# Performance work log

Hardware: AMD Instinct MI355X
Metric: run time of the kernel (lower is better)

## Reference

```python
import jax, jax.numpy as jnp
import numpy as np

CUTOFF = 5.0
EPS = 1e-3  # keras BatchNormalization default epsilon
L = 3       # num_interactions
N = 100000
E = 1600000
H = 64
FIN = 16


def setup_inputs() -> dict:
    key = jax.random.key(0)
    ks = jax.random.split(key, 16)
    s = 0.1  # weight scale for numerical stability
    return {
        "x": jax.random.normal(ks[0], (N, FIN), jnp.float32),
        "edge_index": jax.random.randint(ks[1], (2, E), 0, N, jnp.int32),
        "distances": jax.random.uniform(ks[2], (E,), jnp.float32) * CUTOFF,
        "edge_attr": jax.random.normal(ks[3], (E, 1), jnp.float32),
        "emb_W": jax.random.normal(ks[4], (FIN, H), jnp.float32) * s,
        "emb_b": jnp.zeros((H,), jnp.float32),
        "fW1": jax.random.normal(ks[5], (L, 1, H), jnp.float32) * s,
        "fb1": jnp.zeros((L, H), jnp.float32),
        "fW2": jax.random.normal(ks[6], (L, H, H), jnp.float32) * s,
        "fb2": jnp.zeros((L, H), jnp.float32),
        "iW1": jax.random.normal(ks[7], (L, H, H), jnp.float32) * s,
        "ib1": jnp.zeros((L, H), jnp.float32),
        "iW2": jax.random.normal(ks[8], (L, H, H), jnp.float32) * s,
        "ib2": jnp.zeros((L, H), jnp.float32),
        "bn_gamma": jnp.ones((L, H), jnp.float32),
        "bn_beta": jnp.zeros((L, H), jnp.float32),
        "oW1": jax.random.normal(ks[9], (H, H // 2), jnp.float32) * s,
        "ob1": jnp.zeros((H // 2,), jnp.float32),
        "og1": jnp.ones((H // 2,), jnp.float32),
        "obt1": jnp.zeros((H // 2,), jnp.float32),
        "oW2": jax.random.normal(ks[10], (H // 2, H // 2), jnp.float32) * s,
        "ob2": jnp.zeros((H // 2,), jnp.float32),
        "og2": jnp.ones((H // 2,), jnp.float32),
        "obt2": jnp.zeros((H // 2,), jnp.float32),
        "fin_W": jax.random.normal(ks[11], (H // 2, 3), jnp.float32) * s,
        "fin_b": jnp.zeros((3,), jnp.float32),
    }


def reference(x, edge_index, distances, edge_attr,
              emb_W, emb_b, fW1, fb1, fW2, fb2,
              iW1, ib1, iW2, ib2, bn_gamma, bn_beta,
              oW1, ob1, og1, obt1, oW2, ob2, og2, obt2,
              fin_W, fin_b):
    n_nodes = x.shape[0]
    row, col = edge_index[0], edge_index[1]
    inv = 1.0 / jnp.sqrt(1.0 + EPS)  # BN inference with moving mean=0, var=1

    # shared edge-level quantities
    scaled = distances * (2.0 / CUTOFF) - 1.0                       # [E]
    cut = 0.5 * (jnp.cos(distances * np.pi / CUTOFF) + 1.0)
    cut = jnp.where(distances <= CUTOFF, cut, 0.0)                  # [E]

    h = x @ emb_W + emb_b                                           # [N,H]
    for l in range(L):
        # filter MLP: [E,1] -> [E,F]
        f = jnp.tanh(scaled[:, None] * fW1[l][0] + fb1[l]) @ fW2[l] + fb2[l]
        f = f * cut[:, None]
        # original: sum_F(neighbor[:,None,:] * f[:,:,None]) == neighbor * sum_F(f)
        fs = f.sum(-1)                                              # [E]
        msgs = h[col] * fs[:, None]                                 # [E,H] gather
        agg = jax.ops.segment_sum(msgs, row, num_segments=n_nodes)  # [N,H] scatter-add
        out = jax.nn.softplus(agg @ iW1[l] + ib1[l]) @ iW2[l] + ib2[l]
        out = out * inv * bn_gamma[l] + bn_beta[l]                  # BN (inference)
        h = h + out

    g = h.mean(axis=0)                                              # [H]
    g = jax.nn.softplus(g @ oW1 + ob1) * inv * og1 + obt1
    g = jax.nn.softplus(g @ oW2 + ob2) * inv * og2 + obt2
    return g @ fin_W + fin_b                                        # [3]
```

## Files before the change

kernel.cpp:

```cpp
#include <hip/hip_runtime.h>
#include <hip/hip_fp16.h>
#include <math.h>

#define CUTOFF 5.0f
#define H 64
#define FIN 16
#define NLAYERS 3
#define LUTN 2048
#define LUTSTRIDE 2052
#define ASTRIDE 72
#define MEANB 256
#define BROWS 512
#define NBMAX 256
#define MAXC 10240
#define ABLK 4096

#define BN_INV 0.999500374750f

typedef _Float16 h8 __attribute__((ext_vector_type(8)));
typedef _Float16 h2 __attribute__((ext_vector_type(2)));
typedef float f32x4 __attribute__((ext_vector_type(4)));
typedef unsigned int u32x2 __attribute__((ext_vector_type(2)));

__device__ __forceinline__ float softplus_f(float x) {
    return fmaxf(x, 0.f) + __logf(1.f + __expf(-fabsf(x)));
}

__global__ __launch_bounds__(1024)
void k_pre(const float* __restrict__ x, const float* __restrict__ emb_W,
           const float* __restrict__ emb_b, _Float16* __restrict__ h0,
           const float* __restrict__ fW1, const float* __restrict__ fb1,
           const float* __restrict__ fW2, const float* __restrict__ fb2,
           const float* __restrict__ iW1, const float* __restrict__ iW2,
           const float* __restrict__ bn_g, const float* __restrict__ bn_b,
           const float* __restrict__ ib2, h8* __restrict__ Wsw,
           float* __restrict__ b2p, float* __restrict__ lut,
           unsigned int* __restrict__ cursor, int N, int nbE16) {
    __shared__ float swsum[64];
    __shared__ float sbsum;
    int b = blockIdx.x;
    int t = threadIdx.x;
    if (b < nbE16) {
        int lane = t & 63;
        int w = t >> 6;
        int node = b * 16 + w;
        if (node < N) {
            float acc = emb_b[lane];
#pragma unroll
            for (int k = 0; k < FIN; k++) acc += x[node * FIN + k] * emb_W[k * H + lane];
            h0[(size_t)node * H + lane] = (_Float16)acc;
        }
    } else if (b < nbE16 + NLAYERS * 3) {
        int lb = b - nbE16;
        int l = lb / 3, part = lb % 3;
        if (t < 64) {
            float s = 0.f;
            for (int j = 0; j < H; j++) s += fW2[l * H * H + t * H + j];
            swsum[t] = s;
        }
        if (t == 64) {
            float s = 0.f;
            for (int j = 0; j < H; j++) s += fb2[l * H + j];
            sbsum = s;
        }
        __syncthreads();
        int i = part * 1024 + t;
        if (i <= LUTN) {
            float d = (float)i * (CUTOFF / (float)LUTN);
            float scaled = d * (2.0f / CUTOFF) - 1.0f;
            float cut = 0.5f * (__cosf(d * (3.14159265358979f / CUTOFF)) + 1.0f);
            if (d > CUTOFF) cut = 0.f;
            float s = 0.f;
            for (int hh = 0; hh < H; hh++) {
                int wi = l * H + hh;
                s += tanhf(scaled * fW1[wi] + fb1[wi]) * swsum[hh];
            }
            lut[l * LUTSTRIDE + i] = cut * (s + sbsum);
        }
    } else {
        int tid = (b - nbE16 - NLAYERS * 3) * 1024 + t;
        if (tid < NBMAX) cursor[tid] = (unsigned)tid * MAXC;
        if (tid < NLAYERS * H)
            b2p[tid] = ib2[tid] * BN_INV * bn_g[tid] + bn_b[tid];
        if (tid < NLAYERS * 2 * 8 * 64) {
            int lane = tid & 63;
            int frag = (tid >> 6) & 7;
            int mat  = (tid >> 9) & 1;
            int l    = tid >> 10;
            int kt = frag >> 2, nt = frag & 3;
            int n = nt * 16 + (lane & 15);
            int k0 = kt * 32 + (lane >> 4) * 8;
            const float* W = (mat ? iW2 : iW1) + l * H * H;
            float scale = mat ? BN_INV * bn_g[l * H + n] : 1.0f;
            h8 v;
#pragma unroll
            for (int j = 0; j < 8; j++) v[j] = (_Float16)(W[(k0 + j) * H + n] * scale);
            Wsw[tid] = v;
        }
    }
}

__global__ __launch_bounds__(1024)
void k_passA(const int* __restrict__ ei, const float* __restrict__ dist,
             unsigned int* __restrict__ cursor, u32x2* __restrict__ stg,
             int N, int E, int NB) {
    __shared__ unsigned s_cnt[NBMAX];
    __shared__ unsigned s_base[NBMAX];
    int t = threadIdx.x;
    int e0 = blockIdx.x * ABLK;
    for (int i = t; i < NB; i += 1024) s_cnt[i] = 0;
    __syncthreads();
    int rowv[4];
    unsigned rkv[4] = {0u, 0u, 0u, 0u};
    int bkv[4] = {0, 0, 0, 0};
#pragma unroll
    for (int j = 0; j < 4; j++) {
        int e = e0 + j * 1024 + t;
        rowv[j] = -1;
        if (e < E) {
            int r = ei[e];
            int bk = r / BROWS;
            rkv[j] = atomicAdd(&s_cnt[bk], 1u);
            bkv[j] = bk;
            rowv[j] = r;
        }
    }
    __syncthreads();
    for (int i = t; i < NB; i += 1024)
        s_base[i] = s_cnt[i] ? atomicAdd(&cursor[i], s_cnt[i]) : 0u;
    __syncthreads();
#pragma unroll
    for (int j = 0; j < 4; j++) {
        int e = e0 + j * 1024 + t;
        if (e < E) {
            int col = ei[E + e];
            float d = dist[e];
            int didx = (int)(d * (32768.0f / CUTOFF) + 0.5f);
            didx = max(0, min(didx, 32767));
            unsigned g = s_base[bkv[j]] + rkv[j];
            u32x2 rec;
            rec.x = ((unsigned)col << 15) | (unsigned)didx;
            rec.y = (unsigned)rowv[j];
            if (g < ((unsigned)bkv[j] + 1u) * MAXC)
                stg[g] = rec;
        }
    }
}

__global__ __launch_bounds__(1024)
void k_passB(const u32x2* __restrict__ stg, const unsigned int* __restrict__ cursor,
             int* __restrict__ row_ptr, unsigned int* __restrict__ recs,
             int N, int NB) {
    __shared__ int s_bb[NBMAX];
    __shared__ int s_c[BROWS];
    __shared__ int s_x[BROWS];
    __shared__ unsigned s_out[MAXC];
    int b = blockIdx.x, t = threadIdx.x;
    if (t < NBMAX) {
        int cb = 0;
        if (t < NB) {
            cb = (int)(cursor[t] - (unsigned)t * MAXC);
            cb = min(cb, MAXC);
        }
        s_bb[t] = cb;
    }
    __syncthreads();
    for (int off = 1; off < NBMAX; off <<= 1) {
        int v = 0;
        if (t < NBMAX && t >= off) v = s_bb[t - off];
        __syncthreads();
        if (t < NBMAX) s_bb[t] += v;
        __syncthreads();
    }
    int bbase = (b > 0) ? s_bb[b - 1] : 0;
    int cnt = s_bb[b] - bbase;
    int r0 = b * BROWS;
    int r1 = min(r0 + BROWS, N);
    int nrows = r1 - r0;
    if (t < BROWS) s_c[t] = 0;
    __syncthreads();
    const u32x2* mystg = stg + (size_t)b * MAXC;
    for (int i = t; i < cnt; i += 1024)
        atomicAdd(&s_c[(int)mystg[i].y - r0], 1);
    __syncthreads();
    if (t < BROWS) s_x[t] = s_c[t];
    __syncthreads();
    for (int off = 1; off < BROWS; off <<= 1) {
        int v = 0;
        if (t < BROWS && t >= off) v = s_x[t - off];
        __syncthreads();
        if (t < BROWS) s_x[t] += v;
        __syncthreads();
    }
    if (t < nrows) {
        int excl = s_x[t] - s_c[t];
        row_ptr[r0 + t] = bbase + excl;
        s_c[t] = excl;
    }
    if (b == NB - 1 && t == 0) row_ptr[N] = bbase + cnt;
    __syncthreads();
    for (int i = t; i < cnt; i += 1024) {
        u32x2 rec = mystg[i];
        int slot = atomicAdd(&s_c[(int)rec.y - r0], 1);
        s_out[slot] = rec.x;
    }
    __syncthreads();
    for (int i = t; i < cnt; i += 1024)
        recs[bbase + i] = s_out[i];
}

__global__ __launch_bounds__(256, 8)
void k_layer(const int* __restrict__ row_ptr, const unsigned int* __restrict__ recs,
             const float* __restrict__ lutl, const h8* __restrict__ Wsw,
             const float* __restrict__ b1, const float* __restrict__ b2p,
             const _Float16* __restrict__ h_in, _Float16* __restrict__ h_out,
             int N) {
    __shared__ float s_lut[LUTN + 1];
    __shared__ _Float16 sA[64 * ASTRIDE];
    for (int i = threadIdx.x; i <= LUTN; i += 256) s_lut[i] = lutl[i];
    __syncthreads();

    int lane = threadIdx.x & 63;
    int w = threadIdx.x >> 6;
    int base = blockIdx.x * 64 + w * 16;
    int g = lane >> 3, ci = lane & 7;
    const uint4* h4 = (const uint4*)h_in;

#pragma unroll
    for (int half = 0; half < 2; half++) {
        int node = base + half * 8 + g;
        h2 acc[4];
#pragma unroll
        for (int q = 0; q < 4; q++) acc[q] = (h2){(_Float16)0.f, (_Float16)0.f};
        if (node < N) {
            int s = row_ptr[node], t = row_ptr[node + 1];
            for (int k = s; k < t; k += 4) {
                int k1 = (k + 1 < t) ? k + 1 : k;
                int k2 = (k + 2 < t) ? k + 2 : k;
                int k3 = (k + 3 < t) ? k + 3 : k;
                unsigned r0 = recs[k];
                unsigned r1 = recs[k1];
                unsigned r2 = recs[k2];
                unsigned r3 = recs[k3];
                float td0 = (float)(r0 & 32767u) * (1.0f / 16.0f);
                float td1 = (float)(r1 & 32767u) * (1.0f / 16.0f);
                float td2 = (float)(r2 & 32767u) * (1.0f / 16.0f);
                float td3 = (float)(r3 & 32767u) * (1.0f / 16.0f);
                int i0 = (int)td0, i1 = (int)td1, i2 = (int)td2, i3 = (int)td3;
                float fr0 = td0 - (float)i0, fr1 = td1 - (float)i1;
                float fr2 = td2 - (float)i2, fr3 = td3 - (float)i3;
                float f00 = s_lut[i0], f01 = s_lut[i1];
                float f02 = s_lut[i2], f03 = s_lut[i3];
                float fv0 = f00 + fr0 * (s_lut[i0 + 1] - f00);
                float fv1 = f01 + fr1 * (s_lut[i1 + 1] - f01);
                float fv2 = f02 + fr2 * (s_lut[i2 + 1] - f02);
                float fv3 = f03 + fr3 * (s_lut[i3 + 1] - f03);
                fv1 = (k + 1 < t) ? fv1 : 0.f;
                fv2 = (k + 2 < t) ? fv2 : 0.f;
                fv3 = (k + 3 < t) ? fv3 : 0.f;
                union { uint4 u; h2 v[4]; } p0, p1, p2, p3;
                p0.u = h4[(r0 >> 15) * 8u + (unsigned)ci];
                p1.u = h4[(r1 >> 15) * 8u + (unsigned)ci];
                p2.u = h4[(r2 >> 15) * 8u + (unsigned)ci];
                p3.u = h4[(r3 >> 15) * 8u + (unsigned)ci];
                _Float16 fh0 = (_Float16)fv0, fh1 = (_Float16)fv1;
                _Float16 fh2 = (_Float16)fv2, fh3 = (_Float16)fv3;
                h2 a0 = (h2){fh0, fh0};
                h2 a1 = (h2){fh1, fh1};
                h2 a2 = (h2){fh2, fh2};
                h2 a3 = (h2){fh3, fh3};
#pragma unroll
                for (int q = 0; q < 4; q++) acc[q] += a0 * p0.v[q];
#pragma unroll
                for (int q = 0; q < 4; q++) acc[q] += a1 * p1.v[q];
#pragma unroll
                for (int q = 0; q < 4; q++) acc[q] += a2 * p2.v[q];
#pragma unroll
                for (int q = 0; q < 4; q++) acc[q] += a3 * p3.v[q];
            }
        }
        union { uint4 u4; h2 v[4]; } pk;
#pragma unroll
        for (int q = 0; q < 4; q++) pk.v[q] = acc[q];
        *(uint4*)&sA[(size_t)(w * 16 + half * 8 + g) * ASTRIDE + ci * 8] = pk.u4;
    }

    int q4 = lane >> 4, c16 = lane & 15;
    int rowb = w * 16;
    const h8* WB1 = Wsw;
    const h8* WB2 = Wsw + 8 * 64;
    h8 A0 = *(const h8*)&sA[(size_t)(rowb + c16) * ASTRIDE + q4 * 8];
    h8 A1 = *(const h8*)&sA[(size_t)(rowb + c16) * ASTRIDE + 32 + q4 * 8];
    f32x4 C1[4];
#pragma unroll
    for (int nt = 0; nt < 4; nt++) {
        f32x4 c = {0.f, 0.f, 0.f, 0.f};
        c = __builtin_amdgcn_mfma_f32_16x16x32_f16(A0, WB1[nt * 64 + lane], c, 0, 0, 0);
        c = __builtin_amdgcn_mfma_f32_16x16x32_f16(A1, WB1[(4 + nt) * 64 + lane], c, 0, 0, 0);
        C1[nt] = c;
    }
#pragma unroll
    for (int nt = 0; nt < 4; nt++) {
        float bb = b1[nt * 16 + c16];
#pragma unroll
        for (int reg = 0; reg < 4; reg++) {
            float v = softplus_f(C1[nt][reg] + bb);
            sA[(size_t)(rowb + q4 * 4 + reg) * ASTRIDE + nt * 16 + c16] = (_Float16)v;
        }
    }
    h8 M0 = *(const h8*)&sA[(size_t)(rowb + c16) * ASTRIDE + q4 * 8];
    h8 M1 = *(const h8*)&sA[(size_t)(rowb + c16) * ASTRIDE + 32 + q4 * 8];
    f32x4 C2[4];
#pragma unroll
    for (int nt = 0; nt < 4; nt++) {
        f32x4 c = {0.f, 0.f, 0.f, 0.f};
        c = __builtin_amdgcn_mfma_f32_16x16x32_f16(M0, WB2[nt * 64 + lane], c, 0, 0, 0);
        c = __builtin_amdgcn_mfma_f32_16x16x32_f16(M1, WB2[(4 + nt) * 64 + lane], c, 0, 0, 0);
        C2[nt] = c;
    }
#pragma unroll
    for (int nt = 0; nt < 4; nt++) {
        float bb2 = b2p[nt * 16 + c16];
#pragma unroll
        for (int reg = 0; reg < 4; reg++) {
            int node = base + q4 * 4 + reg;
            if (node < N) {
                size_t idx = (size_t)node * H + nt * 16 + c16;
                float hn = (float)h_in[idx] + C2[nt][reg] + bb2;
                h_out[idx] = (_Float16)hn;
            }
        }
    }
}

__global__ __launch_bounds__(256)
void k_mean(const _Float16* __restrict__ hb, float* __restrict__ partials, int N) {
    __shared__ float s_r[4][H];
    int lane = threadIdx.x & 63;
    int w = threadIdx.x >> 6;
    int wg = blockIdx.x * 4 + w;
    int stride = gridDim.x * 4;
    float local = 0.f;
    for (int i = wg; i < N; i += stride) local += (float)hb[(size_t)i * H + lane];
    s_r[w][lane] = local;
    __syncthreads();
    if (w == 0) {
        float s = s_r[0][lane] + s_r[1][lane] + s_r[2][lane] + s_r[3][lane];
        partials[(size_t)blockIdx.x * H + lane] = s;
    }
}

__global__ __launch_bounds__(256)
void k_final(const float* __restrict__ partials, int N,
             const float* __restrict__ oW1, const float* __restrict__ ob1,
             const float* __restrict__ og1, const float* __restrict__ obt1,
             const float* __restrict__ oW2, const float* __restrict__ ob2,
             const float* __restrict__ og2, const float* __restrict__ obt2,
             const float* __restrict__ fin_W, const float* __restrict__ fin_b,
             float* __restrict__ out) {
    __shared__ float red[4][H];
    __shared__ float sg[H], su[H / 2], sv[H / 2];
    int t = threadIdx.x;
    int ch = t & 63, grp = t >> 6;
    float s = 0.f;
    for (int b = grp; b < MEANB; b += 4) s += partials[(size_t)b * H + ch];
    red[grp][ch] = s;
    __syncthreads();
    if (t < H) sg[t] = (red[0][t] + red[1][t] + red[2][t] + red[3][t]) / (float)N;
    __syncthreads();
    int j = t;
    if (j < H / 2) {
        float acc = ob1[j];
        for (int k = 0; k < H; k++) acc += sg[k] * oW1[k * (H / 2) + j];
        su[j] = softplus_f(acc) * BN_INV * og1[j] + obt1[j];
    }
    __syncthreads();
    if (j < H / 2) {
        float acc = ob2[j];
        for (int k = 0; k < H / 2; k++) acc += su[k] * oW2[k * (H / 2) + j];
        sv[j] = softplus_f(acc) * BN_INV * og2[j] + obt2[j];
    }
    __syncthreads();
    if (j < 3) {
        float acc = fin_b[j];
        for (int k = 0; k < H / 2; k++) acc += sv[k] * fin_W[k * 3 + j];
        out[j] = acc;
    }
}

extern "C" void kernel_launch(void* const* d_in, const int* in_sizes, int n_in,
                              void* d_out, int out_size, void* d_ws, size_t ws_size,
                              hipStream_t stream) {
    const float* x      = (const float*)d_in[0];
    const int*   ei     = (const int*)d_in[1];
    const float* dist   = (const float*)d_in[2];
    const float* emb_W  = (const float*)d_in[4];
    const float* emb_b  = (const float*)d_in[5];
    const float* fW1    = (const float*)d_in[6];
    const float* fb1    = (const float*)d_in[7];
    const float* fW2    = (const float*)d_in[8];
    const float* fb2    = (const float*)d_in[9];
    const float* iW1    = (const float*)d_in[10];
    const float* ib1    = (const float*)d_in[11];
    const float* iW2    = (const float*)d_in[12];
    const float* ib2    = (const float*)d_in[13];
    const float* bn_g   = (const float*)d_in[14];
    const float* bn_b   = (const float*)d_in[15];
    const float* oW1    = (const float*)d_in[16];
    const float* ob1    = (const float*)d_in[17];
    const float* og1    = (const float*)d_in[18];
    const float* obt1   = (const float*)d_in[19];
    const float* oW2    = (const float*)d_in[20];
    const float* ob2    = (const float*)d_in[21];
    const float* og2    = (const float*)d_in[22];
    const float* obt2   = (const float*)d_in[23];
    const float* fin_W  = (const float*)d_in[24];
    const float* fin_b  = (const float*)d_in[25];
    float* out = (float*)d_out;

    int N = in_sizes[0] / FIN;
    int E = in_sizes[2];
    int NB = (N + BROWS - 1) / BROWS;

    float*  ws   = (float*)d_ws;
    _Float16* h0 = (_Float16*)ws;
    _Float16* h1 = h0 + (size_t)N * H;
    unsigned int* recs = (unsigned int*)(h1 + (size_t)N * H);
    h8*     Wsw  = (h8*)(recs + E);
    float*  lut  = (float*)(Wsw + NLAYERS * 2 * 8 * 64);
    float*  partials = lut + 3 * LUTSTRIDE;
    float*  b2p  = partials + MEANB * H;
    u32x2*  stg  = (u32x2*)(b2p + NLAYERS * H);
    int*    row_ptr = (int*)(stg + (size_t)NBMAX * MAXC);
    unsigned int* cursor = (unsigned int*)(row_ptr + N + 1);

    int nbE16 = (N + 15) / 16;
    int nb_pre = nbE16 + NLAYERS * 3 + 3;
    k_pre<<<nb_pre, 1024, 0, stream>>>(x, emb_W, emb_b, h0,
                                       fW1, fb1, fW2, fb2, iW1, iW2,
                                       bn_g, bn_b, ib2, Wsw, b2p, lut,
                                       cursor, N, nbE16);

    int nbA = (E + ABLK - 1) / ABLK;
    k_passA<<<nbA, 1024, 0, stream>>>(ei, dist, cursor, stg, N, E, NB);
    k_passB<<<NB, 1024, 0, stream>>>(stg, cursor, row_ptr, recs, N, NB);

    _Float16* hp[2] = {h0, h1};
    int nb_tile = (N + 63) / 64;
    for (int l = 0; l < NLAYERS; l++) {
        k_layer<<<nb_tile, 256, 0, stream>>>(row_ptr, recs, lut + (size_t)l * LUTSTRIDE,
                                             Wsw + (size_t)l * 1024,
                                             ib1 + l * H, b2p + l * H,
                                             hp[l & 1], hp[(l + 1) & 1], N);
    }
    _Float16* h_final = hp[NLAYERS & 1];

    k_mean<<<MEANB, 256, 0, stream>>>(h_final, partials, N);
    k_final<<<1, 256, 0, stream>>>(partials, N, oW1, ob1, og1, obt1,
                                   oW2, ob2, og2, obt2, fin_W, fin_b, out);
}
```

Before: 339.1 us.

## Fuse edge bucketing into pre kernel, interleave node gathers, fuse final-layer mean

```diff
diff --git a/kernel.cpp b/kernel.cpp
--- a/kernel.cpp
+++ b/kernel.cpp
@@ -35,23 +35,66 @@
            const float* __restrict__ bn_g, const float* __restrict__ bn_b,
            const float* __restrict__ ib2, h8* __restrict__ Wsw,
            float* __restrict__ b2p, float* __restrict__ lut,
-           unsigned int* __restrict__ cursor, int N, int nbE16) {
+           const int* __restrict__ ei, const float* __restrict__ dist,
+           unsigned int* __restrict__ cursor, u32x2* __restrict__ stg,
+           int N, int E, int NB, int nbA, int nbE16) {
+    __shared__ unsigned s_cnt[NBMAX];
+    __shared__ unsigned s_base[NBMAX];
     __shared__ float swsum[64];
     __shared__ float sbsum;
     int b = blockIdx.x;
     int t = threadIdx.x;
-    if (b < nbE16) {
+    if (b < nbA) {
+        int e0 = b * ABLK;
+        for (int i = t; i < NB; i += 1024) s_cnt[i] = 0;
+        __syncthreads();
+        int rowv[4];
+        unsigned rkv[4] = {0u, 0u, 0u, 0u};
+        int bkv[4] = {0, 0, 0, 0};
+#pragma unroll
+        for (int j = 0; j < 4; j++) {
+            int e = e0 + j * 1024 + t;
+            rowv[j] = -1;
+            if (e < E) {
+                int r = ei[e];
+                int bk = r / BROWS;
+                rkv[j] = atomicAdd(&s_cnt[bk], 1u);
+                bkv[j] = bk;
+                rowv[j] = r;
+            }
+        }
+        __syncthreads();
+        for (int i = t; i < NB; i += 1024)
+            s_base[i] = s_cnt[i] ? atomicAdd(&cursor[i], s_cnt[i]) : 0u;
+        __syncthreads();
+#pragma unroll
+        for (int j = 0; j < 4; j++) {
+            int e = e0 + j * 1024 + t;
+            if (e < E) {
+                int col = ei[E + e];
+                float d = dist[e];
+                int didx = (int)(d * (32768.0f / CUTOFF) + 0.5f);
+                didx = max(0, min(didx, 32767));
+                unsigned g = s_base[bkv[j]] + rkv[j];
+                u32x2 rec;
+                rec.x = ((unsigned)col << 15) | (unsigned)didx;
+                rec.y = (unsigned)rowv[j];
+                if (g < MAXC)
+                    stg[(size_t)bkv[j] * MAXC + g] = rec;
+            }
+        }
+    } else if (b < nbA + nbE16) {
         int lane = t & 63;
         int w = t >> 6;
-        int node = b * 16 + w;
+        int node = (b - nbA) * 16 + w;
         if (node < N) {
             float acc = emb_b[lane];
 #pragma unroll
             for (int k = 0; k < FIN; k++) acc += x[node * FIN + k] * emb_W[k * H + lane];
             h0[(size_t)node * H + lane] = (_Float16)acc;
         }
-    } else if (b < nbE16 + NLAYERS * 3) {
-        int lb = b - nbE16;
+    } else if (b < nbA + nbE16 + NLAYERS * 3) {
+        int lb = b - nbA - nbE16;
         int l = lb / 3, part = lb % 3;
         if (t < 64) {
             float s = 0.f;
@@ -78,8 +121,7 @@
             lut[l * LUTSTRIDE + i] = cut * (s + sbsum);
         }
     } else {
-        int tid = (b - nbE16 - NLAYERS * 3) * 1024 + t;
-        if (tid < NBMAX) cursor[tid] = (unsigned)tid * MAXC;
+        int tid = (b - nbA - nbE16 - NLAYERS * 3) * 1024 + t;
         if (tid < NLAYERS * H)
             b2p[tid] = ib2[tid] * BN_INV * bn_g[tid] + bn_b[tid];
         if (tid < NLAYERS * 2 * 8 * 64) {
@@ -101,53 +143,6 @@
 }
 
 __global__ __launch_bounds__(1024)
-void k_passA(const int* __restrict__ ei, const float* __restrict__ dist,
-             unsigned int* __restrict__ cursor, u32x2* __restrict__ stg,
-             int N, int E, int NB) {
-    __shared__ unsigned s_cnt[NBMAX];
-    __shared__ unsigned s_base[NBMAX];
-    int t = threadIdx.x;
-    int e0 = blockIdx.x * ABLK;
-    for (int i = t; i < NB; i += 1024) s_cnt[i] = 0;
-    __syncthreads();
-    int rowv[4];
-    unsigned rkv[4] = {0u, 0u, 0u, 0u};
-    int bkv[4] = {0, 0, 0, 0};
-#pragma unroll
-    for (int j = 0; j < 4; j++) {
-        int e = e0 + j * 1024 + t;
-        rowv[j] = -1;
-        if (e < E) {
-            int r = ei[e];
-            int bk = r / BROWS;
-            rkv[j] = atomicAdd(&s_cnt[bk], 1u);
-            bkv[j] = bk;
-            rowv[j] = r;
-        }
-    }
-    __syncthreads();
-    for (int i = t; i < NB; i += 1024)
-        s_base[i] = s_cnt[i] ? atomicAdd(&cursor[i], s_cnt[i]) : 0u;
-    __syncthreads();
-#pragma unroll
-    for (int j = 0; j < 4; j++) {
-        int e = e0 + j * 1024 + t;
-        if (e < E) {
-            int col = ei[E + e];
-            float d = dist[e];
-            int didx = (int)(d * (32768.0f / CUTOFF) + 0.5f);
-            didx = max(0, min(didx, 32767));
-            unsigned g = s_base[bkv[j]] + rkv[j];
-            u32x2 rec;
-            rec.x = ((unsigned)col << 15) | (unsigned)didx;
-            rec.y = (unsigned)rowv[j];
-            if (g < ((unsigned)bkv[j] + 1u) * MAXC)
-                stg[g] = rec;
-        }
-    }
-}
-
-__global__ __launch_bounds__(1024)
 void k_passB(const u32x2* __restrict__ stg, const unsigned int* __restrict__ cursor,
              int* __restrict__ row_ptr, unsigned int* __restrict__ recs,
              int N, int NB) {
@@ -158,10 +153,7 @@
     int b = blockIdx.x, t = threadIdx.x;
     if (t < NBMAX) {
         int cb = 0;
-        if (t < NB) {
-            cb = (int)(cursor[t] - (unsigned)t * MAXC);
-            cb = min(cb, MAXC);
-        }
+        if (t < NB) cb = min((int)cursor[t], MAXC);
         s_bb[t] = cb;
     }
     __syncthreads();
@@ -177,11 +169,19 @@
     int r0 = b * BROWS;
     int r1 = min(r0 + BROWS, N);
     int nrows = r1 - r0;
+    const u32x2* mystg = stg + (size_t)b * MAXC;
+    u32x2 myrec[10];
+    int nmine = 0;
+#pragma unroll
+    for (int i = 0; i < 10; i++) {
+        int idx = t + i * 1024;
+        if (idx < cnt) { myrec[i] = mystg[idx]; nmine = i + 1; }
+    }
     if (t < BROWS) s_c[t] = 0;
     __syncthreads();
-    const u32x2* mystg = stg + (size_t)b * MAXC;
-    for (int i = t; i < cnt; i += 1024)
-        atomicAdd(&s_c[(int)mystg[i].y - r0], 1);
+#pragma unroll
+    for (int i = 0; i < 10; i++)
+        if (i < nmine) atomicAdd(&s_c[(int)myrec[i].y - r0], 1);
     __syncthreads();
     if (t < BROWS) s_x[t] = s_c[t];
     __syncthreads();
@@ -199,22 +199,63 @@
     }
     if (b == NB - 1 && t == 0) row_ptr[N] = bbase + cnt;
     __syncthreads();
-    for (int i = t; i < cnt; i += 1024) {
-        u32x2 rec = mystg[i];
-        int slot = atomicAdd(&s_c[(int)rec.y - r0], 1);
-        s_out[slot] = rec.x;
-    }
+#pragma unroll
+    for (int i = 0; i < 10; i++)
+        if (i < nmine) {
+            int slot = atomicAdd(&s_c[(int)myrec[i].y - r0], 1);
+            s_out[slot] = myrec[i].x;
+        }
     __syncthreads();
     for (int i = t; i < cnt; i += 1024)
         recs[bbase + i] = s_out[i];
 }
 
-__global__ __launch_bounds__(256, 8)
+#define PROC4(KK, SS, TT, ACC) do {                                          \
+    int _lim = ((TT) > (SS)) ? (TT) - 1 : 0;                                 \
+    int _ka = min((KK), _lim),     _kb = min((KK) + 1, _lim);                \
+    int _kc = min((KK) + 2, _lim), _kd = min((KK) + 3, _lim);                \
+    unsigned _ra = recs[_ka], _rb = recs[_kb];                               \
+    unsigned _rc = recs[_kc], _rd = recs[_kd];                               \
+    float _ta = (float)(_ra & 32767u) * (1.0f / 16.0f);                      \
+    float _tb = (float)(_rb & 32767u) * (1.0f / 16.0f);                      \
+    float _tc = (float)(_rc & 32767u) * (1.0f / 16.0f);                      \
+    float _td = (float)(_rd & 32767u) * (1.0f / 16.0f);                      \
+    int _ia = (int)_ta, _ib = (int)_tb, _ic = (int)_tc, _id = (int)_td;      \
+    float _fa = s_lut[_ia], _fb = s_lut[_ib];                                \
+    float _fc = s_lut[_ic], _fd = s_lut[_id];                                \
+    float _va = _fa + (_ta - (float)_ia) * (s_lut[_ia + 1] - _fa);           \
+    float _vb = _fb + (_tb - (float)_ib) * (s_lut[_ib + 1] - _fb);           \
+    float _vc = _fc + (_tc - (float)_ic) * (s_lut[_ic + 1] - _fc);           \
+    float _vd = _fd + (_td - (float)_id) * (s_lut[_id + 1] - _fd);           \
+    _va = ((KK)     < (TT)) ? _va : 0.f;                                     \
+    _vb = ((KK) + 1 < (TT)) ? _vb : 0.f;                                     \
+    _vc = ((KK) + 2 < (TT)) ? _vc : 0.f;                                     \
+    _vd = ((KK) + 3 < (TT)) ? _vd : 0.f;                                     \
+    union { uint4 u; h2 v[4]; } _pa, _pb, _pc, _pd;                          \
+    _pa.u = h4[(_ra >> 15) * 8u + (unsigned)ci];                             \
+    _pb.u = h4[(_rb >> 15) * 8u + (unsigned)ci];                             \
+    _pc.u = h4[(_rc >> 15) * 8u + (unsigned)ci];                             \
+    _pd.u = h4[(_rd >> 15) * 8u + (unsigned)ci];                             \
+    _Float16 _ha = (_Float16)_va, _hb = (_Float16)_vb;                       \
+    _Float16 _hc = (_Float16)_vc, _hd = (_Float16)_vd;                       \
+    h2 _aa = (h2){_ha, _ha}, _ab = (h2){_hb, _hb};                           \
+    h2 _ac = (h2){_hc, _hc}, _ad = (h2){_hd, _hd};                           \
+    _Pragma("unroll")                                                        \
+    for (int _q = 0; _q < 4; _q++) (ACC)[_q] += _aa * _pa.v[_q];             \
+    _Pragma("unroll")                                                        \
+    for (int _q = 0; _q < 4; _q++) (ACC)[_q] += _ab * _pb.v[_q];             \
+    _Pragma("unroll")                                                        \
+    for (int _q = 0; _q < 4; _q++) (ACC)[_q] += _ac * _pc.v[_q];             \
+    _Pragma("unroll")                                                        \
+    for (int _q = 0; _q < 4; _q++) (ACC)[_q] += _ad * _pd.v[_q];             \
+} while (0)
+
+__global__ __launch_bounds__(256, 6)
 void k_layer(const int* __restrict__ row_ptr, const unsigned int* __restrict__ recs,
              const float* __restrict__ lutl, const h8* __restrict__ Wsw,
              const float* __restrict__ b1, const float* __restrict__ b2p,
              const _Float16* __restrict__ h_in, _Float16* __restrict__ h_out,
-             int N) {
+             float* __restrict__ pA, int N, int last) {
     __shared__ float s_lut[LUTN + 1];
     __shared__ _Float16 sA[64 * ASTRIDE];
     for (int i = threadIdx.x; i <= LUTN; i += 256) s_lut[i] = lutl[i];
@@ -226,63 +267,34 @@
     int g = lane >> 3, ci = lane & 7;
     const uint4* h4 = (const uint4*)h_in;
 
-#pragma unroll
-    for (int half = 0; half < 2; half++) {
-        int node = base + half * 8 + g;
-        h2 acc[4];
-#pragma unroll
-        for (int q = 0; q < 4; q++) acc[q] = (h2){(_Float16)0.f, (_Float16)0.f};
-        if (node < N) {
-            int s = row_ptr[node], t = row_ptr[node + 1];
-            for (int k = s; k < t; k += 4) {
-                int k1 = (k + 1 < t) ? k + 1 : k;
-                int k2 = (k + 2 < t) ? k + 2 : k;
-                int k3 = (k + 3 < t) ? k + 3 : k;
-                unsigned r0 = recs[k];
-                unsigned r1 = recs[k1];
-                unsigned r2 = recs[k2];
-                unsigned r3 = recs[k3];
-                float td0 = (float)(r0 & 32767u) * (1.0f / 16.0f);
-                float td1 = (float)(r1 & 32767u) * (1.0f / 16.0f);
-                float td2 = (float)(r2 & 32767u) * (1.0f / 16.0f);
-                float td3 = (float)(r3 & 32767u) * (1.0f / 16.0f);
-                int i0 = (int)td0, i1 = (int)td1, i2 = (int)td2, i3 = (int)td3;
-                float fr0 = td0 - (float)i0, fr1 = td1 - (float)i1;
-                float fr2 = td2 - (float)i2, fr3 = td3 - (float)i3;
-                float f00 = s_lut[i0], f01 = s_lut[i1];
-                float f02 = s_lut[i2], f03 = s_lut[i3];
-                float fv0 = f00 + fr0 * (s_lut[i0 + 1] - f00);
-                float fv1 = f01 + fr1 * (s_lut[i1 + 1] - f01);
-                float fv2 = f02 + fr2 * (s_lut[i2 + 1] - f02);
-                float fv3 = f03 + fr3 * (s_lut[i3 + 1] - f03);
-                fv1 = (k + 1 < t) ? fv1 : 0.f;
-                fv2 = (k + 2 < t) ? fv2 : 0.f;
-                fv3 = (k + 3 < t) ? fv3 : 0.f;
-                union { uint4 u; h2 v[4]; } p0, p1, p2, p3;
-                p0.u = h4[(r0 >> 15) * 8u + (unsigned)ci];
-                p1.u = h4[(r1 >> 15) * 8u + (unsigned)ci];
-                p2.u = h4[(r2 >> 15) * 8u + (unsigned)ci];
-                p3.u = h4[(r3 >> 15) * 8u + (unsigned)ci];
-                _Float16 fh0 = (_Float16)fv0, fh1 = (_Float16)fv1;
-                _Float16 fh2 = (_Float16)fv2, fh3 = (_Float16)fv3;
-                h2 a0 = (h2){fh0, fh0};
-                h2 a1 = (h2){fh1, fh1};
-                h2 a2 = (h2){fh2, fh2};
-                h2 a3 = (h2){fh3, fh3};
-#pragma unroll
-                for (int q = 0; q < 4; q++) acc[q] += a0 * p0.v[q];
-#pragma unroll
-                for (int q = 0; q < 4; q++) acc[q] += a1 * p1.v[q];
-#pragma unroll
-                for (int q = 0; q < 4; q++) acc[q] += a2 * p2.v[q];
-#pragma unroll
-                for (int q = 0; q < 4; q++) acc[q] += a3 * p3.v[q];
-            }
+    {
+        int node0 = base + g;
+        int node1 = base + 8 + g;
+        h2 acc0[4], acc1[4];
+#pragma unroll
+        for (int q = 0; q < 4; q++) {
+            acc0[q] = (h2){(_Float16)0.f, (_Float16)0.f};
+            acc1[q] = (h2){(_Float16)0.f, (_Float16)0.f};
+        }
+        int s0 = 0, t0 = 0, s1 = 0, t1 = 0;
+        if (node0 < N) { s0 = row_ptr[node0]; t0 = row_ptr[node0 + 1]; }
+        if (node1 < N) { s1 = row_ptr[node1]; t1 = row_ptr[node1 + 1]; }
+        int it0 = (t0 - s0 + 3) >> 2;
+        int it1 = (t1 - s1 + 3) >> 2;
+        int iters = max(it0, it1);
+        for (int it = 0; it < iters; ++it) {
+            int k0 = s0 + it * 4;
+            int k1 = s1 + it * 4;
+            PROC4(k0, s0, t0, acc0);
+            PROC4(k1, s1, t1, acc1);
         }
         union { uint4 u4; h2 v[4]; } pk;
 #pragma unroll
-        for (int q = 0; q < 4; q++) pk.v[q] = acc[q];
-        *(uint4*)&sA[(size_t)(w * 16 + half * 8 + g) * ASTRIDE + ci * 8] = pk.u4;
+        for (int q = 0; q < 4; q++) pk.v[q] = acc0[q];
+        *(uint4*)&sA[(size_t)(w * 16 + g) * ASTRIDE + ci * 8] = pk.u4;
+#pragma unroll
+        for (int q = 0; q < 4; q++) pk.v[q] = acc1[q];
+        *(uint4*)&sA[(size_t)(w * 16 + 8 + g) * ASTRIDE + ci * 8] = pk.u4;
     }
 
     int q4 = lane >> 4, c16 = lane & 15;
@@ -318,30 +330,56 @@
         c = __builtin_amdgcn_mfma_f32_16x16x32_f16(M1, WB2[(4 + nt) * 64 + lane], c, 0, 0, 0);
         C2[nt] = c;
     }
-#pragma unroll
-    for (int nt = 0; nt < 4; nt++) {
-        float bb2 = b2p[nt * 16 + c16];
-#pragma unroll
-        for (int reg = 0; reg < 4; reg++) {
-            int node = base + q4 * 4 + reg;
-            if (node < N) {
-                size_t idx = (size_t)node * H + nt * 16 + c16;
-                float hn = (float)h_in[idx] + C2[nt][reg] + bb2;
-                h_out[idx] = (_Float16)hn;
+    if (!last) {
+#pragma unroll
+        for (int nt = 0; nt < 4; nt++) {
+            float bb2 = b2p[nt * 16 + c16];
+#pragma unroll
+            for (int reg = 0; reg < 4; reg++) {
+                int node = base + q4 * 4 + reg;
+                if (node < N) {
+                    size_t idx = (size_t)node * H + nt * 16 + c16;
+                    float hn = (float)h_in[idx] + C2[nt][reg] + bb2;
+                    h_out[idx] = (_Float16)hn;
+                }
             }
         }
+    } else {
+        float ps[4];
+#pragma unroll
+        for (int nt = 0; nt < 4; nt++) {
+            float bb2 = b2p[nt * 16 + c16];
+            float s = 0.f;
+#pragma unroll
+            for (int reg = 0; reg < 4; reg++) {
+                int node = base + q4 * 4 + reg;
+                if (node < N) {
+                    size_t idx = (size_t)node * H + nt * 16 + c16;
+                    s += (float)h_in[idx] + C2[nt][reg] + bb2;
+                }
+            }
+            ps[nt] = s;
+        }
+#pragma unroll
+        for (int nt = 0; nt < 4; nt++) {
+            float v = ps[nt];
+            v += __shfl_xor(v, 16, 64);
+            v += __shfl_xor(v, 32, 64);
+            if (lane < 16)
+                pA[((size_t)blockIdx.x * 4 + w) * H + nt * 16 + c16] = v;
+        }
     }
 }
 
 __global__ __launch_bounds__(256)
-void k_mean(const _Float16* __restrict__ hb, float* __restrict__ partials, int N) {
+void k_mean(const float* __restrict__ pA, float* __restrict__ partials, int P) {
     __shared__ float s_r[4][H];
     int lane = threadIdx.x & 63;
     int w = threadIdx.x >> 6;
     int wg = blockIdx.x * 4 + w;
     int stride = gridDim.x * 4;
     float local = 0.f;
-    for (int i = wg; i < N; i += stride) local += (float)hb[(size_t)i * H + lane];
+    for (int i = wg; i < P; i += stride) local += pA[(size_t)i * H + lane];
     s_r[w][lane] = local;
     __syncthreads();
     if (w == 0) {
@@ -421,6 +459,8 @@
     int N = in_sizes[0] / FIN;
     int E = in_sizes[2];
     int NB = (N + BROWS - 1) / BROWS;
+    int nb_tile = (N + 63) / 64;
+    int P = nb_tile * 4;
 
     float*  ws   = (float*)d_ws;
     _Float16* h0 = (_Float16*)ws;
@@ -430,32 +470,34 @@
     float*  lut  = (float*)(Wsw + NLAYERS * 2 * 8 * 64);
     float*  partials = lut + 3 * LUTSTRIDE;
     float*  b2p  = partials + MEANB * H;
-    u32x2*  stg  = (u32x2*)(b2p + NLAYERS * H);
+    float*  pA   = b2p + NLAYERS * H;
+    u32x2*  stg  = (u32x2*)(pA + (size_t)P * H);
     int*    row_ptr = (int*)(stg + (size_t)NBMAX * MAXC);
     unsigned int* cursor = (unsigned int*)(row_ptr + N + 1);
 
+    hipMemsetAsync(cursor, 0, NBMAX * sizeof(unsigned int), stream);
+
+    int nbA = (E + ABLK - 1) / ABLK;
     int nbE16 = (N + 15) / 16;
-    int nb_pre = nbE16 + NLAYERS * 3 + 3;
+    int nb_pre = nbA + nbE16 + NLAYERS * 3 + 3;
     k_pre<<<nb_pre, 1024, 0, stream>>>(x, emb_W, emb_b, h0,
                                        fW1, fb1, fW2, fb2, iW1, iW2,
                                        bn_g, bn_b, ib2, Wsw, b2p, lut,
-                                       cursor, N, nbE16);
-
-    int nbA = (E + ABLK - 1) / ABLK;
-    k_passA<<<nbA, 1024, 0, stream>>>(ei, dist, cursor, stg, N, E, NB);
+                                       ei, dist, cursor, stg,
+                                       N, E, NB, nbA, nbE16);
+
     k_passB<<<NB, 1024, 0, stream>>>(stg, cursor, row_ptr, recs, N, NB);
 
     _Float16* hp[2] = {h0, h1};
-    int nb_tile = (N + 63) / 64;
     for (int l = 0; l < NLAYERS; l++) {
         k_layer<<<nb_tile, 256, 0, stream>>>(row_ptr, recs, lut + (size_t)l * LUTSTRIDE,
                                              Wsw + (size_t)l * 1024,
                                              ib1 + l * H, b2p + l * H,
-                                             hp[l & 1], hp[(l + 1) & 1], N);
-    }
-    _Float16* h_final = hp[NLAYERS & 1];
-
-    k_mean<<<MEANB, 256, 0, stream>>>(h_final, partials, N);
+                                             hp[l & 1], hp[(l + 1) & 1], pA, N,
+                                             (l == NLAYERS - 1) ? 1 : 0);
+    }
+
+    k_mean<<<MEANB, 256, 0, stream>>>(pA, partials, P);
     k_final<<<1, 256, 0, stream>>>(partials, N, oW1, ob1, og1, obt1,
                                    oW2, ob2, og2, obt2, fin_W, fin_b, out);
 }
```

New measurement: 331.5 us. -2.3%, faster.
